# Kernel tuning notes

Hardware: AMD Instinct MI355X
Metric: run time of the kernel (lower is better)

The kernel has to match this reference:

```python
import jax, jax.numpy as jnp
import numpy as np

EPS = 1e-5
NUM_GROUPS = 32
NUM_HEADS = 4


def setup_inputs() -> dict:
    key = jax.random.key(0)
    ks = jax.random.split(key, 7)
    b, c, h, w = 4, 256, 64, 64
    x = jax.random.normal(ks[0], (b, c, h, w), dtype=jnp.float32)
    gn_w = jax.random.normal(ks[1], (c,), dtype=jnp.float32) * 0.02 + 1.0
    gn_b = jax.random.normal(ks[2], (c,), dtype=jnp.float32) * 0.02
    qkv_w = jax.random.normal(ks[3], (3 * c, c), dtype=jnp.float32) * (1.0 / np.sqrt(c))
    qkv_b = jax.random.normal(ks[4], (3 * c,), dtype=jnp.float32) * 0.02
    proj_w = jax.random.normal(ks[5], (c, c), dtype=jnp.float32) * (1.0 / np.sqrt(c))
    proj_b = jax.random.normal(ks[6], (c,), dtype=jnp.float32) * 0.02
    return {"x": x, "gn_w": gn_w, "gn_b": gn_b, "qkv_w": qkv_w,
            "qkv_b": qkv_b, "proj_w": proj_w, "proj_b": proj_b}


def _group_norm(x, w, b):
    # GroupNorm32: compute in float32, cast back to input dtype
    bsz, c, h, ww = x.shape
    xf = x.astype(jnp.float32).reshape(bsz, NUM_GROUPS, c // NUM_GROUPS, h, ww)
    mean = xf.mean(axis=(2, 3, 4), keepdims=True)
    var = xf.var(axis=(2, 3, 4), keepdims=True)
    xn = (xf - mean) * jax.lax.rsqrt(var + EPS)
    xn = xn.reshape(bsz, c, h, ww)
    xn = xn * w[None, :, None, None] + b[None, :, None, None]
    return xn.astype(x.dtype)


def reference(x, gn_w, gn_b, qkv_w, qkv_b, proj_w, proj_b):
    b, c, h, w = x.shape
    hd = c // NUM_HEADS
    n = h * w
    xn = _group_norm(x, gn_w, gn_b)
    # 1x1 conv == per-pixel linear: [b, 3c, h, w]
    qkv = jnp.einsum('oc,bchw->bohw', qkv_w, xn) + qkv_b[None, :, None, None]
    qkv = qkv.reshape(b, 3, NUM_HEADS, hd, n)
    q, k, v = qkv[:, 0], qkv[:, 1], qkv[:, 2]  # [b, H, hd, n]
    scale = hd ** -0.5
    # scores [b, H, n, n]
    attn = jnp.einsum('bhdq,bhdk->bhqk', q, k) * scale
    attn = jax.nn.softmax(attn, axis=-1)
    out = jnp.einsum('bhqk,bhdk->bhdq', attn, v)  # [b, H, hd, n]
    out = out.reshape(b, c, h, w)
    out = jnp.einsum('oc,bchw->bohw', proj_w, out) + proj_b[None, :, None, None]
    return x + out
```

## Files before the change

### kernel.cpp

```cpp
#include <hip/hip_runtime.h>

typedef __attribute__((ext_vector_type(8))) short bfrag;
typedef __attribute__((ext_vector_type(4))) float ffrag;
typedef __attribute__((ext_vector_type(8))) unsigned short us8;
typedef __attribute__((ext_vector_type(4))) unsigned short us4;
typedef __attribute__((ext_vector_type(2))) unsigned short us2;

#define DEVI static __device__ __forceinline__

DEVI unsigned short f2bf(float f){
  unsigned int u = __float_as_uint(f);
  u += 0x7fffu + ((u >> 16) & 1u);
  return (unsigned short)(u >> 16);
}
DEVI float fexp2(float x){ float r; asm("v_exp_f32 %0, %1" : "=v"(r) : "v"(x)); return r; }
DEVI unsigned int cvt_pk_bf16(float lo, float hi){
  unsigned int r;
  asm("v_cvt_pk_bf16_f32 %0, %1, %2" : "=v"(r) : "v"(lo), "v"(hi));
  return r;
}
DEVI int swz64(int r, int c){ return ((r << 6) + c) ^ ((r & 7) << 3); }
DEVI int swz256(int r, int c){ return ((r << 8) + c) ^ ((r & 7) << 3); }

DEVI void gload16(const unsigned short* g, unsigned short* l){
  __builtin_amdgcn_global_load_lds(
      (const __attribute__((address_space(1))) unsigned int*)g,
      (__attribute__((address_space(3))) unsigned int*)l, 16, 0, 0);
}

__global__ __launch_bounds__(256) void prep_gn(
    const float* __restrict__ x, const float* __restrict__ gw,
    const float* __restrict__ gb, const float* __restrict__ qkvw,
    const float* __restrict__ qkvb, const float* __restrict__ pw,
    unsigned short* __restrict__ wq, unsigned short* __restrict__ wp,
    float* __restrict__ bq, unsigned short* __restrict__ xnt){
  __shared__ float ps[4], pq[4];
  if (blockIdx.x >= 128){
    const int i = (blockIdx.x - 128) * 256 + threadIdx.x;
    const float qs = 0.125f * 1.44269504f;
    if (i < 49152){
      float4 v = ((const float4*)qkvw)[i];
      float sc = (i < 16384) ? qs : 1.f;
      us4 u; u[0]=f2bf(v.x*sc); u[1]=f2bf(v.y*sc); u[2]=f2bf(v.z*sc); u[3]=f2bf(v.w*sc);
      ((us4*)wq)[i] = u;
    }
    if (i < 16384){
      float4 v = ((const float4*)pw)[i];
      us4 u; u[0]=f2bf(v.x); u[1]=f2bf(v.y); u[2]=f2bf(v.z); u[3]=f2bf(v.w);
      ((us4*)wp)[i] = u;
    }
    if (i < 768) bq[i] = qkvb[i] * (i < 256 ? qs : 1.f);
    return;
  }
  const int b = blockIdx.x >> 5, g = blockIdx.x & 31;
  const int t = threadIdx.x;
  const float* xb = x + (((size_t)b * 256 + g * 8) << 12);
  float s = 0.f, q = 0.f;
  #pragma unroll
  for (int c = 0; c < 8; ++c){
    const float4* base = (const float4*)(xb + ((size_t)c << 12));
    #pragma unroll
    for (int e = 0; e < 4; ++e){
      float4 v = base[e * 256 + t];
      s += v.x + v.y + v.z + v.w;
      q += v.x * v.x + v.y * v.y + v.z * v.z + v.w * v.w;
    }
  }
  #pragma unroll
  for (int m = 32; m; m >>= 1){ s += __shfl_down(s, m); q += __shfl_down(q, m); }
  if ((t & 63) == 0){ ps[t >> 6] = s; pq[t >> 6] = q; }
  __syncthreads();
  float S = ps[0] + ps[1] + ps[2] + ps[3];
  float Q = pq[0] + pq[1] + pq[2] + pq[3];
  float mean = S * (1.f / 32768.f);
  float var  = Q * (1.f / 32768.f) - mean * mean;
  float rstd = rsqrtf(var + 1e-5f);
  float sc[8], sh[8];
  #pragma unroll
  for (int c = 0; c < 8; ++c){
    sc[c] = gw[g * 8 + c] * rstd;
    sh[c] = gb[g * 8 + c] - mean * sc[c];
  }
  unsigned short* dst = xnt + (((size_t)b << 12) << 8) + (g << 3);
  #pragma unroll
  for (int e = 0; e < 16; ++e){
    const int n = e * 256 + t;
    us8 u;
    #pragma unroll
    for (int c = 0; c < 8; ++c)
      u[c] = f2bf(xb[((size_t)c << 12) + n] * sc[c] + sh[c]);
    *(us8*)(dst + ((size_t)n << 8)) = u;
  }
}

__global__ __launch_bounds__(256) void qkv_gemm(
    const unsigned short* __restrict__ xnt, const unsigned short* __restrict__ W,
    const float* __restrict__ bias, unsigned short* __restrict__ qt,
    unsigned short* __restrict__ kt, unsigned short* __restrict__ vt){
  const int n0 = blockIdx.x << 6, MT = blockIdx.y, b = blockIdx.z;
  const int t = threadIdx.x, l = t & 63, w = t >> 6;
  __shared__ __align__(16) unsigned short AB[32768];
  unsigned short* Al = AB;
  unsigned short* Bl = AB + 16384;
  const unsigned short* Asrc = W + (size_t)(MT << 6) * 256;
  const unsigned short* Bsrc = xnt + ((((size_t)b << 12) + n0) << 8);
  #pragma unroll
  for (int e = 0; e < 8; ++e){
    const int idx = e * 256 + t;
    const int r = idx >> 5, g = idx & 31;
    const int gs = (g ^ (r & 7)) << 3;
    unsigned short* db = &AB[(e * 256 + (w << 6)) << 3];
    gload16(Asrc + (r << 8) + gs, db);
    gload16(Bsrc + (r << 8) + gs, db + 16384);
  }
  __syncthreads();
  ffrag acc[4] = {{0,0,0,0},{0,0,0,0},{0,0,0,0},{0,0,0,0}};
  #pragma unroll
  for (int kc = 0; kc < 8; ++kc){
    bfrag a = *(const bfrag*)&Al[swz256((w << 4) + (l & 15), (kc << 5) + ((l >> 4) << 3))];
    #pragma unroll
    for (int fc = 0; fc < 4; ++fc){
      bfrag bb = *(const bfrag*)&Bl[swz256((fc << 4) + (l & 15), (kc << 5) + ((l >> 4) << 3))];
      acc[fc] = __builtin_amdgcn_mfma_f32_16x16x32_bf16(a, bb, acc[fc], 0, 0, 0);
    }
  }
  const int which = MT >> 2, h = MT & 3;
  const int d0 = (w << 4) + ((l >> 4) << 2);
  float bi[4];
  #pragma unroll
  for (int r = 0; r < 4; ++r) bi[r] = bias[(MT << 6) + d0 + r];
  #pragma unroll
  for (int fc = 0; fc < 4; ++fc){
    int n = n0 + (fc << 4) + (l & 15);
    if (which < 2){
      unsigned short* dst = (which == 0 ? qt : kt) +
          (((size_t)(b * 4 + h)) << 18) + ((size_t)n << 6) + d0;
      us4 u;
      #pragma unroll
      for (int r = 0; r < 4; ++r) u[r] = f2bf(acc[fc][r] + bi[r]);
      *(us4*)dst = u;
    } else {
      const int np = n0 + ((fc & 2) << 4) + (((l >> 2) & 3) << 3)
                        + ((fc & 1) << 2) + (l & 3);
      #pragma unroll
      for (int r = 0; r < 4; ++r)
        vt[((((size_t)(b * 4 + h)) << 6) + d0 + r) * 4096 + np] = f2bf(acc[fc][r] + bi[r]);
    }
  }
}

__global__ __launch_bounds__(512, 4) void attn_kernel(
    const unsigned short* __restrict__ qt, const unsigned short* __restrict__ kt,
    const unsigned short* __restrict__ vt, unsigned short* __restrict__ at){
  const int id = blockIdx.x;
  const int xc = id & 7, k2 = id >> 3;
  const int bhid = (xc << 1) + (k2 >> 5);
  const int qx = k2 & 31;
  const int b = bhid >> 2, h = bhid & 3;
  const int q0 = qx << 7;
  const int t = threadIdx.x, l = t & 63, w = t >> 6;
  const int wq = w & 3, kh = w >> 2;
  const size_t bh = (size_t)bhid;
  __shared__ __align__(16) unsigned short S[32768];
  const unsigned short* kbase = kt + (bh << 18);
  const unsigned short* vbase = vt + (bh << 18);

  const int row = t >> 3;
  const int gx = ((t & 7) ^ (row & 7)) << 3;
  const int koff = (row << 6) + gx;
  unsigned short* ldst = &S[w << 9];
  const unsigned short* qsrc = qt + (bh << 18) + ((size_t)q0 << 6);
  gload16(qsrc + koff, ldst + 8192);
  gload16(qsrc + 4096 + koff, ldst + 12288);
  gload16(kbase + koff, ldst);
  gload16(vbase + (row << 12) + gx, ldst + 16384);
  gload16(kbase + 4096 + koff, ldst + 4096);
  gload16(vbase + (row << 12) + 64 + gx, ldst + 20480);
  asm volatile("s_waitcnt vmcnt(4)" ::: "memory");
  __builtin_amdgcn_s_barrier();
  __builtin_amdgcn_sched_barrier(0);
  const int qreg = (wq >> 1) ? 12288 : 8192;
  const int qrow = ((wq & 1) << 5) + (l & 15);
  bfrag bq00 = *(const bfrag*)&S[qreg + swz64(qrow,      (l >> 4) << 3)];
  bfrag bq01 = *(const bfrag*)&S[qreg + swz64(qrow, 32 + ((l >> 4) << 3))];
  bfrag bq10 = *(const bfrag*)&S[qreg + swz64(qrow + 16,      (l >> 4) << 3)];
  bfrag bq11 = *(const bfrag*)&S[qreg + swz64(qrow + 16, 32 + ((l >> 4) << 3))];
  asm volatile("s_waitcnt lgkmcnt(0)" ::: "memory");
  asm volatile("s_waitcnt vmcnt(2)" ::: "memory");
  __builtin_amdgcn_s_barrier();
  __builtin_amdgcn_sched_barrier(0);

  ffrag acc[2][4] = {{{0,0,0,0},{0,0,0,0},{0,0,0,0},{0,0,0,0}},
                     {{0,0,0,0},{0,0,0,0},{0,0,0,0},{0,0,0,0}}};
  ffrag zs[2] = {{0,0,0,0},{0,0,0,0}};
  const ffrag zf = {0.f, 0.f, 0.f, 0.f};
  bfrag onesB;
  #pragma unroll
  for (int j = 0; j < 8; ++j) onesB[j] = (short)0x3F80;
  union uA { bfrag bb; unsigned int u[4]; };
  uA A0p, A1p;

  auto body = [&](int kbr, int vbrp, bool dopv) __attribute__((always_inline)) {
    ffrag s[2][2];
    #pragma unroll
    for (int j = 0; j < 2; ++j){
      const int fc = (kh << 1) + j;
      bfrag ak0 = *(const bfrag*)&S[kbr + swz64((fc << 4) + (l & 15), (l >> 4) << 3)];
      bfrag ak1 = *(const bfrag*)&S[kbr + swz64((fc << 4) + (l & 15), 32 + ((l >> 4) << 3))];
      ffrag z0 = __builtin_amdgcn_mfma_f32_16x16x32_bf16(ak0, bq00, zf, 0, 0, 0);
      z0 = __builtin_amdgcn_mfma_f32_16x16x32_bf16(ak1, bq01, z0, 0, 0, 0);
      ffrag z1 = __builtin_amdgcn_mfma_f32_16x16x32_bf16(ak0, bq10, zf, 0, 0, 0);
      z1 = __builtin_amdgcn_mfma_f32_16x16x32_bf16(ak1, bq11, z1, 0, 0, 0);
      s[0][j] = z0; s[1][j] = z1;
    }
    if (dopv){
      zs[0] = __builtin_amdgcn_mfma_f32_16x16x32_bf16(A0p.bb, onesB, zs[0], 0, 0, 0);
      zs[1] = __builtin_amdgcn_mfma_f32_16x16x32_bf16(A1p.bb, onesB, zs[1], 0, 0, 0);
      #pragma unroll
      for (int fc = 0; fc < 4; ++fc){
        bfrag vv = *(const bfrag*)&S[vbrp + swz64((fc << 4) + (l & 15),
                                                 (kh << 5) + ((l >> 4) << 3))];
        acc[0][fc] = __builtin_amdgcn_mfma_f32_16x16x32_bf16(A0p.bb, vv, acc[0][fc], 0, 0, 0);
        acc[1][fc] = __builtin_amdgcn_mfma_f32_16x16x32_bf16(A1p.bb, vv, acc[1][fc], 0, 0, 0);
      }
    }
    float p[2][2][4];
    #pragma unroll
    for (int g = 0; g < 2; ++g){
      #pragma unroll
      for (int j = 0; j < 2; ++j){
        #pragma unroll
        for (int r = 0; r < 4; ++r) p[g][j][r] = fexp2(s[g][j][r]);
      }
    }
    A0p.u[0] = cvt_pk_bf16(p[0][0][0], p[0][0][1]); A0p.u[1] = cvt_pk_bf16(p[0][0][2], p[0][0][3]);
    A0p.u[2] = cvt_pk_bf16(p[0][1][0], p[0][1][1]); A0p.u[3] = cvt_pk_bf16(p[0][1][2], p[0][1][3]);
    A1p.u[0] = cvt_pk_bf16(p[1][0][0], p[1][0][1]); A1p.u[1] = cvt_pk_bf16(p[1][0][2], p[1][0][3]);
    A1p.u[2] = cvt_pk_bf16(p[1][1][0], p[1][1][1]); A1p.u[3] = cvt_pk_bf16(p[1][1][2], p[1][1][3]);
  };
  auto issue2 = [&](int kti2, int buf) __attribute__((always_inline)) {
    gload16(kbase + (kti2 << 12) + koff, ldst + (buf << 12));
    gload16(vbase + (row << 12) + (kti2 << 6) + gx, ldst + 16384 + (buf << 12));
  };

#define ATTN_STEP(KTI, BUF)                                               \
    issue2((KTI) + 2, ((BUF) + 2) & 3);                                   \
    body((BUF) << 12, 16384 + (((((BUF) + 3) & 3)) << 12), true);         \
    asm volatile("s_waitcnt vmcnt(2)" ::: "memory");                      \
    __builtin_amdgcn_s_barrier();                                         \
    __builtin_amdgcn_sched_barrier(0);

  issue2(2, 2);
  body(0, 16384, false);
  asm volatile("s_waitcnt vmcnt(2)" ::: "memory");
  __builtin_amdgcn_s_barrier();
  __builtin_amdgcn_sched_barrier(0);
  for (int base = 1; base < 61; base += 4){
    ATTN_STEP(base + 0, 1)
    ATTN_STEP(base + 1, 2)
    ATTN_STEP(base + 2, 3)
    ATTN_STEP(base + 3, 0)
  }
  ATTN_STEP(61, 1)
  body(2 << 12, 16384 + (1 << 12), true);
  asm volatile("s_waitcnt vmcnt(0)" ::: "memory");
  __builtin_amdgcn_s_barrier();
  __builtin_amdgcn_sched_barrier(0);
  body(3 << 12, 16384 + (2 << 12), true);
  zs[0] = __builtin_amdgcn_mfma_f32_16x16x32_bf16(A0p.bb, onesB, zs[0], 0, 0, 0);
  zs[1] = __builtin_amdgcn_mfma_f32_16x16x32_bf16(A1p.bb, onesB, zs[1], 0, 0, 0);
  #pragma unroll
  for (int fc = 0; fc < 4; ++fc){
    bfrag vv = *(const bfrag*)&S[16384 + (3 << 12) + swz64((fc << 4) + (l & 15),
                                             (kh << 5) + ((l >> 4) << 3))];
    acc[0][fc] = __builtin_amdgcn_mfma_f32_16x16x32_bf16(A0p.bb, vv, acc[0][fc], 0, 0, 0);
    acc[1][fc] = __builtin_amdgcn_mfma_f32_16x16x32_bf16(A1p.bb, vv, acc[1][fc], 0, 0, 0);
  }
#undef ATTN_STEP

  __syncthreads();
  float* Sf = (float*)S;
  if (kh == 1 && (l & 15) == 0){
    #pragma unroll
    for (int g = 0; g < 2; ++g){
      #pragma unroll
      for (int r = 0; r < 4; ++r)
        Sf[8192 + (wq << 5) + (g << 4) + ((l >> 4) << 2) + r] = zs[g][r];
    }
  }
  __syncthreads();
  float inv[2][4];
  if (kh == 0){
    #pragma unroll
    for (int g = 0; g < 2; ++g){
      #pragma unroll
      for (int r = 0; r < 4; ++r)
        inv[g][r] = 1.f / (zs[g][r] +
            Sf[8192 + (wq << 5) + (g << 4) + ((l >> 4) << 2) + r]);
    }
  }
  __syncthreads();
  if (kh == 1){
    #pragma unroll
    for (int g = 0; g < 2; ++g){
      #pragma unroll
      for (int fc = 0; fc < 4; ++fc){
        #pragma unroll
        for (int r = 0; r < 4; ++r)
          Sf[((wq << 5) + (g << 4) + ((l >> 4) << 2) + r) * 64 + (fc << 4) + (l & 15)] =
              acc[g][fc][r];
      }
    }
  }
  __syncthreads();
  if (kh == 0){
    #pragma unroll
    for (int g = 0; g < 2; ++g){
      #pragma unroll
      for (int fc = 0; fc < 4; ++fc){
        #pragma unroll
        for (int r = 0; r < 4; ++r){
          const int ql = (wq << 5) + (g << 4) + ((l >> 4) << 2) + r;
          float ob = Sf[ql * 64 + (fc << 4) + (l & 15)];
          float v = (acc[g][fc][r] + ob) * inv[g][r];
          at[((((size_t)b << 12) + q0 + ql) << 8) + (h << 6) + (fc << 4) + (l & 15)] =
              f2bf(v);
        }
      }
    }
  }
}

__global__ __launch_bounds__(256) void proj_gemm(
    const unsigned short* __restrict__ at, const unsigned short* __restrict__ W,
    const float* __restrict__ bias, const float* __restrict__ x,
    float* __restrict__ out){
  const int n0 = blockIdx.x << 6, MT = blockIdx.y, b = blockIdx.z;
  const int t = threadIdx.x, l = t & 63, w = t >> 6;
  __shared__ __align__(16) unsigned short AB[32768];
  unsigned short* Al = AB;
  unsigned short* Bl = AB + 16384;
  const unsigned short* Asrc = W + (size_t)(MT << 6) * 256;
  const unsigned short* Bsrc = at + ((((size_t)b << 12) + n0) << 8);
  #pragma unroll
  for (int e = 0; e < 8; ++e){
    const int idx = e * 256 + t;
    const int r = idx >> 5, g = idx & 31;
    const int gs = (g ^ (r & 7)) << 3;
    unsigned short* db = &AB[(e * 256 + (w << 6)) << 3];
    gload16(Asrc + (r << 8) + gs, db);
    gload16(Bsrc + (r << 8) + gs, db + 16384);
  }
  __syncthreads();
  ffrag acc[4] = {{0,0,0,0},{0,0,0,0},{0,0,0,0},{0,0,0,0}};
  #pragma unroll
  for (int kc = 0; kc < 8; ++kc){
    bfrag a = *(const bfrag*)&Al[swz256((w << 4) + (l & 15), (kc << 5) + ((l >> 4) << 3))];
    #pragma unroll
    for (int fc = 0; fc < 4; ++fc){
      bfrag bb = *(const bfrag*)&Bl[swz256((fc << 4) + (l & 15), (kc << 5) + ((l >> 4) << 3))];
      acc[fc] = __builtin_amdgcn_mfma_f32_16x16x32_bf16(a, bb, acc[fc], 0, 0, 0);
    }
  }
  const int co = (MT << 6) + (w << 4) + ((l >> 4) << 2);
  #pragma unroll
  for (int fc = 0; fc < 4; ++fc){
    int n = n0 + (fc << 4) + (l & 15);
    #pragma unroll
    for (int r = 0; r < 4; ++r){
      size_t o = (((size_t)b * 256 + co + r) << 12) + n;
      out[o] = acc[fc][r] + bias[co + r] + x[o];
    }
  }
}

extern "C" void kernel_launch(void* const* d_in, const int* in_sizes, int n_in,
                              void* d_out, int out_size, void* d_ws, size_t ws_size,
                              hipStream_t stream){
  const float* x    = (const float*)d_in[0];
  const float* gw   = (const float*)d_in[1];
  const float* gb   = (const float*)d_in[2];
  const float* qkvw = (const float*)d_in[3];
  const float* qkvb = (const float*)d_in[4];
  const float* pw   = (const float*)d_in[5];
  const float* pb   = (const float*)d_in[6];
  float* out = (float*)d_out;

  unsigned short* xnt = (unsigned short*)((char*)d_ws + 16384);
  unsigned short* qt  = xnt + (size_t)4 * 4096 * 256;
  unsigned short* kt  = qt  + (size_t)16 * 4096 * 64;
  unsigned short* vt  = kt  + (size_t)16 * 4096 * 64;
  unsigned short* at  = vt  + (size_t)16 * 4096 * 64;
  unsigned short* wq  = at  + (size_t)4 * 4096 * 256;
  unsigned short* wp  = wq  + (size_t)768 * 256;
  float*          bq  = (float*)(wp + (size_t)256 * 256);

  prep_gn    <<<384, 256, 0, stream>>>(x, gw, gb, qkvw, qkvb, pw, wq, wp, bq, xnt);
  qkv_gemm   <<<dim3(64, 12, 4), 256, 0, stream>>>(xnt, wq, bq, qt, kt, vt);
  attn_kernel<<<dim3(512), 512, 0, stream>>>(qt, kt, vt, at);
  proj_gemm  <<<dim3(64, 4, 4), 256, 0, stream>>>(at, wp, pb, x, out);
}
```

Measured before the change: 118.6 us.

## Drop software-pipelined PV skew, add MFMA priority hints, halve attention loop barriers

Removes the one-iteration skew in which each tile's P·V MFMAs ran during the next tile's QK step, so each body now computes scores, exponentials and P·V on the same tile. MFMA sections are wrapped in s_setprio to raise wave priority during matrix work. Tiles are processed in pairs with a workgroup barrier only after every second tile, halving barrier count. The change loses the intra-wave overlap of exp/convert with independent MFMAs, relying on cross-wave interleaving instead. Skipping the barrier between tiles risks buffer reuse hazards if the 4-buffer prefetch distance is insufficient.

```diff
diff --git a/kernel.cpp b/kernel.cpp
--- a/kernel.cpp
+++ b/kernel.cpp
@@ -197,11 +197,10 @@
   bfrag onesB;
   #pragma unroll
   for (int j = 0; j < 8; ++j) onesB[j] = (short)0x3F80;
-  union uA { bfrag bb; unsigned int u[4]; };
-  uA A0p, A1p;
-
-  auto body = [&](int kbr, int vbrp, bool dopv) __attribute__((always_inline)) {
+
+  auto body = [&](int kbr, int vbr) __attribute__((always_inline)) {
     ffrag s[2][2];
+    __builtin_amdgcn_s_setprio(1);
     #pragma unroll
     for (int j = 0; j < 2; ++j){
       const int fc = (kh << 1) + j;
@@ -213,17 +212,7 @@
       z1 = __builtin_amdgcn_mfma_f32_16x16x32_bf16(ak1, bq11, z1, 0, 0, 0);
       s[0][j] = z0; s[1][j] = z1;
     }
-    if (dopv){
-      zs[0] = __builtin_amdgcn_mfma_f32_16x16x32_bf16(A0p.bb, onesB, zs[0], 0, 0, 0);
-      zs[1] = __builtin_amdgcn_mfma_f32_16x16x32_bf16(A1p.bb, onesB, zs[1], 0, 0, 0);
-      #pragma unroll
-      for (int fc = 0; fc < 4; ++fc){
-        bfrag vv = *(const bfrag*)&S[vbrp + swz64((fc << 4) + (l & 15),
-                                                 (kh << 5) + ((l >> 4) << 3))];
-        acc[0][fc] = __builtin_amdgcn_mfma_f32_16x16x32_bf16(A0p.bb, vv, acc[0][fc], 0, 0, 0);
-        acc[1][fc] = __builtin_amdgcn_mfma_f32_16x16x32_bf16(A1p.bb, vv, acc[1][fc], 0, 0, 0);
-      }
-    }
+    __builtin_amdgcn_s_setprio(0);
     float p[2][2][4];
     #pragma unroll
     for (int g = 0; g < 2; ++g){
@@ -233,50 +222,49 @@
         for (int r = 0; r < 4; ++r) p[g][j][r] = fexp2(s[g][j][r]);
       }
     }
-    A0p.u[0] = cvt_pk_bf16(p[0][0][0], p[0][0][1]); A0p.u[1] = cvt_pk_bf16(p[0][0][2], p[0][0][3]);
-    A0p.u[2] = cvt_pk_bf16(p[0][1][0], p[0][1][1]); A0p.u[3] = cvt_pk_bf16(p[0][1][2], p[0][1][3]);
-    A1p.u[0] = cvt_pk_bf16(p[1][0][0], p[1][0][1]); A1p.u[1] = cvt_pk_bf16(p[1][0][2], p[1][0][3]);
-    A1p.u[2] = cvt_pk_bf16(p[1][1][0], p[1][1][1]); A1p.u[3] = cvt_pk_bf16(p[1][1][2], p[1][1][3]);
+    union { bfrag bb; unsigned int u[4]; } A0, A1;
+    A0.u[0] = cvt_pk_bf16(p[0][0][0], p[0][0][1]); A0.u[1] = cvt_pk_bf16(p[0][0][2], p[0][0][3]);
+    A0.u[2] = cvt_pk_bf16(p[0][1][0], p[0][1][1]); A0.u[3] = cvt_pk_bf16(p[0][1][2], p[0][1][3]);
+    A1.u[0] = cvt_pk_bf16(p[1][0][0], p[1][0][1]); A1.u[1] = cvt_pk_bf16(p[1][0][2], p[1][0][3]);
+    A1.u[2] = cvt_pk_bf16(p[1][1][0], p[1][1][1]); A1.u[3] = cvt_pk_bf16(p[1][1][2], p[1][1][3]);
+    __builtin_amdgcn_s_setprio(1);
+    zs[0] = __builtin_amdgcn_mfma_f32_16x16x32_bf16(A0.bb, onesB, zs[0], 0, 0, 0);
+    zs[1] = __builtin_amdgcn_mfma_f32_16x16x32_bf16(A1.bb, onesB, zs[1], 0, 0, 0);
+    #pragma unroll
+    for (int fc = 0; fc < 4; ++fc){
+      bfrag vv = *(const bfrag*)&S[vbr + swz64((fc << 4) + (l & 15),
+                                              (kh << 5) + ((l >> 4) << 3))];
+      acc[0][fc] = __builtin_amdgcn_mfma_f32_16x16x32_bf16(A0.bb, vv, acc[0][fc], 0, 0, 0);
+      acc[1][fc] = __builtin_amdgcn_mfma_f32_16x16x32_bf16(A1.bb, vv, acc[1][fc], 0, 0, 0);
+    }
+    __builtin_amdgcn_s_setprio(0);
   };
   auto issue2 = [&](int kti2, int buf) __attribute__((always_inline)) {
     gload16(kbase + (kti2 << 12) + koff, ldst + (buf << 12));
     gload16(vbase + (row << 12) + (kti2 << 6) + gx, ldst + 16384 + (buf << 12));
   };
 
-#define ATTN_STEP(KTI, BUF)                                               \
-    issue2((KTI) + 2, ((BUF) + 2) & 3);                                   \
-    body((BUF) << 12, 16384 + (((((BUF) + 3) & 3)) << 12), true);         \
-    asm volatile("s_waitcnt vmcnt(2)" ::: "memory");                      \
-    __builtin_amdgcn_s_barrier();                                         \
+#define ATTN_PAIR(KE, BE, BO)                                 \
+    issue2((KE) + 2, ((BE) + 2) & 3);                         \
+    body((BE) << 12, 16384 + ((BE) << 12));                   \
+    asm volatile("s_waitcnt vmcnt(2)" ::: "memory");          \
+    __builtin_amdgcn_sched_barrier(0);                        \
+    issue2((KE) + 3, ((BO) + 2) & 3);                         \
+    body((BO) << 12, 16384 + ((BO) << 12));                   \
+    asm volatile("s_waitcnt vmcnt(2)" ::: "memory");          \
+    __builtin_amdgcn_s_barrier();                             \
     __builtin_amdgcn_sched_barrier(0);
 
-  issue2(2, 2);
-  body(0, 16384, false);
-  asm volatile("s_waitcnt vmcnt(2)" ::: "memory");
-  __builtin_amdgcn_s_barrier();
+  for (int base = 0; base < 60; base += 4){
+    ATTN_PAIR(base + 0, 0, 1)
+    ATTN_PAIR(base + 2, 2, 3)
+  }
+  ATTN_PAIR(60, 0, 1)
+  body(2 << 12, 16384 + (2 << 12));
+  asm volatile("s_waitcnt vmcnt(0)" ::: "memory");
   __builtin_amdgcn_sched_barrier(0);
-  for (int base = 1; base < 61; base += 4){
-    ATTN_STEP(base + 0, 1)
-    ATTN_STEP(base + 1, 2)
-    ATTN_STEP(base + 2, 3)
-    ATTN_STEP(base + 3, 0)
-  }
-  ATTN_STEP(61, 1)
-  body(2 << 12, 16384 + (1 << 12), true);
-  asm volatile("s_waitcnt vmcnt(0)" ::: "memory");
-  __builtin_amdgcn_s_barrier();
-  __builtin_amdgcn_sched_barrier(0);
-  body(3 << 12, 16384 + (2 << 12), true);
-  zs[0] = __builtin_amdgcn_mfma_f32_16x16x32_bf16(A0p.bb, onesB, zs[0], 0, 0, 0);
-  zs[1] = __builtin_amdgcn_mfma_f32_16x16x32_bf16(A1p.bb, onesB, zs[1], 0, 0, 0);
-  #pragma unroll
-  for (int fc = 0; fc < 4; ++fc){
-    bfrag vv = *(const bfrag*)&S[16384 + (3 << 12) + swz64((fc << 4) + (l & 15),
-                                             (kh << 5) + ((l >> 4) << 3))];
-    acc[0][fc] = __builtin_amdgcn_mfma_f32_16x16x32_bf16(A0p.bb, vv, acc[0][fc], 0, 0, 0);
-    acc[1][fc] = __builtin_amdgcn_mfma_f32_16x16x32_bf16(A1p.bb, vv, acc[1][fc], 0, 0, 0);
-  }
-#undef ATTN_STEP
+  body(3 << 12, 16384 + (3 << 12));
+#undef ATTN_PAIR
 
   __syncthreads();
   float* Sf = (float*)S;
```

Measured after the change: 113.5 us. 1.04x faster.
